# Kernel optimization log

Measured on AMD Instinct MI355X. Metric: run time of the kernel, lower is better.

## Reference

```python
import jax, jax.numpy as jnp
import numpy as np


def setup_inputs() -> dict:
    key = jax.random.key(0)
    ks = jax.random.split(key, 8)
    B, S, H = 8, 2048, 1024
    rep = jax.random.normal(ks[0], (B, S, H), dtype=jnp.float32)
    mask = jax.random.randint(ks[1], (B, S), 0, 2, dtype=jnp.int32)
    Ws = jax.random.normal(ks[2], (H, 2), dtype=jnp.float32) * 0.02
    bs = jax.random.normal(ks[3], (2,), dtype=jnp.float32) * 0.02
    We = jax.random.normal(ks[4], (H, 2), dtype=jnp.float32) * 0.02
    be = jax.random.normal(ks[5], (2,), dtype=jnp.float32) * 0.02
    Wm = jax.random.normal(ks[6], (4, 1), dtype=jnp.float32)
    bm = jax.random.normal(ks[7], (1,), dtype=jnp.float32)
    return {"rep": rep, "mask": mask, "Ws": Ws, "bs": bs, "We": We, "be": be, "Wm": Wm, "bm": bm}


def reference(rep, mask, Ws, bs, We, be, Wm, bm):
    # rep: [B,S,H]; start/end logits: [B,S,2]
    start_logits = rep @ Ws + bs
    end_logits = rep @ We + be
    maskb = mask != 0
    # candidate starts/ends: masked positions where logit[1] >= logit[0]
    start_cand = maskb & (start_logits[..., 0] <= start_logits[..., 1])  # [B,S]
    end_cand = maskb & (end_logits[..., 0] <= end_logits[..., 1])        # [B,S]
    # pair score m(cat(start_logits[b,s], end_logits[b,e])) decomposes additively
    w_start, w_end = Wm[:2, 0], Wm[2:, 0]
    score_s = start_logits @ w_start  # [B,S]
    score_e = end_logits @ w_end      # [B,S]
    pair_score = score_s[:, :, None] + score_e[:, None, :] + bm[0]  # [B,S,S]
    S = rep.shape[1]
    tri = jnp.arange(S)[:, None] <= jnp.arange(S)[None, :]  # s <= e
    valid = (start_cand[:, :, None] & end_cand[:, None, :] & tri & (pair_score > 0))  # [B,S,S]
    masked_scores = jnp.where(valid, pair_score, 0.0)
    return valid, masked_scores
```

## Files before the change

### kernel.cpp

```cpp
#include <hip/hip_runtime.h>

#define BB 8
#define SS 2048
#define HH 1024

__global__ __launch_bounds__(256) void token_kernel(
    const float* __restrict__ rep, const int* __restrict__ mask,
    const float* __restrict__ Ws, const float* __restrict__ bs,
    const float* __restrict__ We, const float* __restrict__ be,
    const float* __restrict__ Wm, const float* __restrict__ bm,
    float* __restrict__ ss, float* __restrict__ se)
{
    const int token = blockIdx.x * 4 + (threadIdx.x >> 6);
    const int lane  = threadIdx.x & 63;
    const float* r = rep + (size_t)token * HH;

    double a0 = 0.0, a1 = 0.0, a2 = 0.0, a3 = 0.0;
    #pragma unroll
    for (int k = 0; k < HH / 256; ++k) {
        const int h = k * 256 + lane * 4;
        const float4 rv = *(const float4*)(r + h);
        const float4 w0 = *(const float4*)(Ws + 2 * h);
        const float4 w1 = *(const float4*)(Ws + 2 * h + 4);
        const float4 e0 = *(const float4*)(We + 2 * h);
        const float4 e1 = *(const float4*)(We + 2 * h + 4);
        a0 += (double)rv.x * w0.x + (double)rv.y * w0.z + (double)rv.z * w1.x + (double)rv.w * w1.z;
        a1 += (double)rv.x * w0.y + (double)rv.y * w0.w + (double)rv.z * w1.y + (double)rv.w * w1.w;
        a2 += (double)rv.x * e0.x + (double)rv.y * e0.z + (double)rv.z * e1.x + (double)rv.w * e1.z;
        a3 += (double)rv.x * e0.y + (double)rv.y * e0.w + (double)rv.z * e1.y + (double)rv.w * e1.w;
    }
    #pragma unroll
    for (int off = 32; off >= 1; off >>= 1) {
        a0 += __shfl_down(a0, off);
        a1 += __shfl_down(a1, off);
        a2 += __shfl_down(a2, off);
        a3 += __shfl_down(a3, off);
    }
    if (lane == 0) {
        const double sl0 = a0 + (double)bs[0];
        const double sl1 = a1 + (double)bs[1];
        const double el0 = a2 + (double)be[0];
        const double el1 = a3 + (double)be[1];
        const bool m  = (mask[token] != 0);
        const bool sc = m && (sl0 <= sl1);
        const bool ec = m && (el0 <= el1);
        const double sv = sl0 * (double)Wm[0] + sl1 * (double)Wm[1];
        const double ev = el0 * (double)Wm[2] + el1 * (double)Wm[3];
        ss[token] = sc ? (float)sv : -1e30f;
        se[token] = ec ? (float)ev : -1e30f;
    }
}

__global__ __launch_bounds__(256) void pair_kernel(
    const float* __restrict__ ss, const float* __restrict__ se,
    const float* __restrict__ bm,
    float* __restrict__ out_valid, float* __restrict__ out_score)
{
    const int b = blockIdx.z;
    const int i = blockIdx.y;
    const int j = (blockIdx.x * 256 + threadIdx.x) * 4;

    const float s_i = ss[b * SS + i];
    const float4 e  = *(const float4*)(se + b * SS + j);
    const float bmv = bm[0];

    const float p0 = (s_i + e.x) + bmv;
    const float p1 = (s_i + e.y) + bmv;
    const float p2 = (s_i + e.z) + bmv;
    const float p3 = (s_i + e.w) + bmv;

    const bool v0 = (i <= j    ) && (p0 > 0.0f);
    const bool v1 = (i <= j + 1) && (p1 > 0.0f);
    const bool v2 = (i <= j + 2) && (p2 > 0.0f);
    const bool v3 = (i <= j + 3) && (p3 > 0.0f);

    const float4 vv = make_float4(v0 ? 1.0f : 0.0f, v1 ? 1.0f : 0.0f,
                                  v2 ? 1.0f : 0.0f, v3 ? 1.0f : 0.0f);
    const float4 pv = make_float4(v0 ? p0 : 0.0f, v1 ? p1 : 0.0f,
                                  v2 ? p2 : 0.0f, v3 ? p3 : 0.0f);

    const size_t off = ((size_t)b * SS + i) * SS + j;
    *(float4*)(out_valid + off) = vv;
    *(float4*)(out_score + off) = pv;
}

extern "C" void kernel_launch(void* const* d_in, const int* in_sizes, int n_in,
                              void* d_out, int out_size, void* d_ws, size_t ws_size,
                              hipStream_t stream) {
    const float* rep  = (const float*)d_in[0];
    const int*   mask = (const int*)  d_in[1];
    const float* Ws   = (const float*)d_in[2];
    const float* bs   = (const float*)d_in[3];
    const float* We   = (const float*)d_in[4];
    const float* be   = (const float*)d_in[5];
    const float* Wm   = (const float*)d_in[6];
    const float* bm   = (const float*)d_in[7];

    float* ss = (float*)d_ws;
    float* se = ss + BB * SS;

    float* out_valid = (float*)d_out;
    float* out_score = out_valid + (size_t)BB * SS * SS;

    token_kernel<<<BB * SS / 4, 256, 0, stream>>>(rep, mask, Ws, bs, We, be,
                                                  Wm, bm, ss, se);

    dim3 g2(SS / 1024, SS, BB);
    pair_kernel<<<g2, 256, 0, stream>>>(ss, se, bm, out_valid, out_score);
}
```

Before: 326.4 us.

## Multi-row pair tiles with nontemporal stores and register-cached weights in token kernel

The pair kernel now has each block cover 8 full rows: each thread loads 8 end scores once and writes 8 columns per row with nontemporal vector stores. This cuts block count and keeps the large streaming output from polluting caches. The token kernel has each wave handle 4 tokens, with the projection weights kept in registers and reused across them. The cost is higher register pressure and fewer blocks for latency hiding.

```diff
diff --git a/kernel.cpp b/kernel.cpp
--- a/kernel.cpp
+++ b/kernel.cpp
@@ -3,6 +3,8 @@
 #define BB 8
 #define SS 2048
 #define HH 1024
+
+typedef float vf4 __attribute__((ext_vector_type(4)));
 
 __global__ __launch_bounds__(256) void token_kernel(
     const float* __restrict__ rep, const int* __restrict__ mask,
@@ -11,43 +13,56 @@
     const float* __restrict__ Wm, const float* __restrict__ bm,
     float* __restrict__ ss, float* __restrict__ se)
 {
-    const int token = blockIdx.x * 4 + (threadIdx.x >> 6);
-    const int lane  = threadIdx.x & 63;
-    const float* r = rep + (size_t)token * HH;
+    const int wave = threadIdx.x >> 6;
+    const int lane = threadIdx.x & 63;
+    const int tok0 = blockIdx.x * 16 + wave * 4;
 
-    double a0 = 0.0, a1 = 0.0, a2 = 0.0, a3 = 0.0;
+    float4 w0[4], w1[4], e0[4], e1[4];
     #pragma unroll
-    for (int k = 0; k < HH / 256; ++k) {
+    for (int k = 0; k < 4; ++k) {
         const int h = k * 256 + lane * 4;
-        const float4 rv = *(const float4*)(r + h);
-        const float4 w0 = *(const float4*)(Ws + 2 * h);
-        const float4 w1 = *(const float4*)(Ws + 2 * h + 4);
-        const float4 e0 = *(const float4*)(We + 2 * h);
-        const float4 e1 = *(const float4*)(We + 2 * h + 4);
-        a0 += (double)rv.x * w0.x + (double)rv.y * w0.z + (double)rv.z * w1.x + (double)rv.w * w1.z;
-        a1 += (double)rv.x * w0.y + (double)rv.y * w0.w + (double)rv.z * w1.y + (double)rv.w * w1.w;
-        a2 += (double)rv.x * e0.x + (double)rv.y * e0.z + (double)rv.z * e1.x + (double)rv.w * e1.z;
-        a3 += (double)rv.x * e0.y + (double)rv.y * e0.w + (double)rv.z * e1.y + (double)rv.w * e1.w;
+        w0[k] = *(const float4*)(Ws + 2 * h);
+        w1[k] = *(const float4*)(Ws + 2 * h + 4);
+        e0[k] = *(const float4*)(We + 2 * h);
+        e1[k] = *(const float4*)(We + 2 * h + 4);
     }
+
     #pragma unroll
-    for (int off = 32; off >= 1; off >>= 1) {
-        a0 += __shfl_down(a0, off);
-        a1 += __shfl_down(a1, off);
-        a2 += __shfl_down(a2, off);
-        a3 += __shfl_down(a3, off);
-    }
-    if (lane == 0) {
-        const double sl0 = a0 + (double)bs[0];
-        const double sl1 = a1 + (double)bs[1];
-        const double el0 = a2 + (double)be[0];
-        const double el1 = a3 + (double)be[1];
-        const bool m  = (mask[token] != 0);
-        const bool sc = m && (sl0 <= sl1);
-        const bool ec = m && (el0 <= el1);
-        const double sv = sl0 * (double)Wm[0] + sl1 * (double)Wm[1];
-        const double ev = el0 * (double)Wm[2] + el1 * (double)Wm[3];
-        ss[token] = sc ? (float)sv : -1e30f;
-        se[token] = ec ? (float)ev : -1e30f;
+    for (int t = 0; t < 4; ++t) {
+        const int token = tok0 + t;
+        const float* r = rep + (size_t)token * HH;
+
+        double a0 = 0.0, a1 = 0.0, a2 = 0.0, a3 = 0.0;
+        #pragma unroll
+        for (int k = 0; k < 4; ++k) {
+            const float4 rv = *(const float4*)(r + k * 256 + lane * 4);
+            a0 += (double)rv.x * w0[k].x + (double)rv.y * w0[k].z + (double)rv.z * w1[k].x + (double)rv.w * w1[k].z;
+            a1 += (double)rv.x * w0[k].y + (double)rv.y * w0[k].w + (double)rv.z * w1[k].y + (double)rv.w * w1[k].w;
+            a2 += (double)rv.x * e0[k].x + (double)rv.y * e0[k].z + (double)rv.z * e1[k].x + (double)rv.w * e1[k].z;
+            a3 += (double)rv.x * e0[k].y + (double)rv.y * e0[k].w + (double)rv.z * e1[k].y + (double)rv.w * e1[k].w;
+        }
+
+        #pragma unroll
+        for (int off = 32; off >= 1; off >>= 1) {
+            a0 += __shfl_down(a0, off);
+            a1 += __shfl_down(a1, off);
+            a2 += __shfl_down(a2, off);
+            a3 += __shfl_down(a3, off);
+        }
+
+        if (lane == 0) {
+            const double sl0 = a0 + (double)bs[0];
+            const double sl1 = a1 + (double)bs[1];
+            const double el0 = a2 + (double)be[0];
+            const double el1 = a3 + (double)be[1];
+            const bool m  = (mask[token] != 0);
+            const bool sc = m && (sl0 <= sl1);
+            const bool ec = m && (el0 <= el1);
+            const double sv = sl0 * (double)Wm[0] + sl1 * (double)Wm[1];
+            const double ev = el0 * (double)Wm[2] + el1 * (double)Wm[3];
+            ss[token] = sc ? (float)sv : -1e30f;
+            se[token] = ec ? (float)ev : -1e30f;
+        }
     }
 }
 
@@ -56,32 +71,40 @@
     const float* __restrict__ bm,
     float* __restrict__ out_valid, float* __restrict__ out_score)
 {
-    const int b = blockIdx.z;
-    const int i = blockIdx.y;
-    const int j = (blockIdx.x * 256 + threadIdx.x) * 4;
-
-    const float s_i = ss[b * SS + i];
-    const float4 e  = *(const float4*)(se + b * SS + j);
+    const int row0 = blockIdx.x * 8;
+    const int b    = row0 >> 11;
+    const int j0   = threadIdx.x * 8;
     const float bmv = bm[0];
 
-    const float p0 = (s_i + e.x) + bmv;
-    const float p1 = (s_i + e.y) + bmv;
-    const float p2 = (s_i + e.z) + bmv;
-    const float p3 = (s_i + e.w) + bmv;
+    const float4 e0 = *(const float4*)(se + b * SS + j0);
+    const float4 e1 = *(const float4*)(se + b * SS + j0 + 4);
+    const float ev[8] = {e0.x, e0.y, e0.z, e0.w, e1.x, e1.y, e1.z, e1.w};
 
-    const bool v0 = (i <= j    ) && (p0 > 0.0f);
-    const bool v1 = (i <= j + 1) && (p1 > 0.0f);
-    const bool v2 = (i <= j + 2) && (p2 > 0.0f);
-    const bool v3 = (i <= j + 3) && (p3 > 0.0f);
+    #pragma unroll
+    for (int r = 0; r < 8; ++r) {
+        const int row = row0 + r;
+        const int i   = row & (SS - 1);
+        const float s_i = ss[row];
 
-    const float4 vv = make_float4(v0 ? 1.0f : 0.0f, v1 ? 1.0f : 0.0f,
-                                  v2 ? 1.0f : 0.0f, v3 ? 1.0f : 0.0f);
-    const float4 pv = make_float4(v0 ? p0 : 0.0f, v1 ? p1 : 0.0f,
-                                  v2 ? p2 : 0.0f, v3 ? p3 : 0.0f);
+        float va[8], pa[8];
+        #pragma unroll
+        for (int c = 0; c < 8; ++c) {
+            const float p = (s_i + ev[c]) + bmv;
+            const bool  v = (i <= j0 + c) && (p > 0.0f);
+            va[c] = v ? 1.0f : 0.0f;
+            pa[c] = v ? p    : 0.0f;
+        }
 
-    const size_t off = ((size_t)b * SS + i) * SS + j;
-    *(float4*)(out_valid + off) = vv;
-    *(float4*)(out_score + off) = pv;
+        const size_t off = (size_t)row * SS + j0;
+        vf4 vv0 = {va[0], va[1], va[2], va[3]};
+        vf4 vv1 = {va[4], va[5], va[6], va[7]};
+        vf4 pv0 = {pa[0], pa[1], pa[2], pa[3]};
+        vf4 pv1 = {pa[4], pa[5], pa[6], pa[7]};
+        __builtin_nontemporal_store(vv0, (vf4*)(out_valid + off));
+        __builtin_nontemporal_store(vv1, (vf4*)(out_valid + off + 4));
+        __builtin_nontemporal_store(pv0, (vf4*)(out_score + off));
+        __builtin_nontemporal_store(pv1, (vf4*)(out_score + off + 4));
+    }
 }
 
 extern "C" void kernel_launch(void* const* d_in, const int* in_sizes, int n_in,
@@ -102,9 +125,9 @@
     float* out_valid = (float*)d_out;
     float* out_score = out_valid + (size_t)BB * SS * SS;
 
-    token_kernel<<<BB * SS / 4, 256, 0, stream>>>(rep, mask, Ws, bs, We, be,
-                                                  Wm, bm, ss, se);
+    token_kernel<<<BB * SS / 16, 256, 0, stream>>>(rep, mask, Ws, bs, We, be,
+                                                   Wm, bm, ss, se);
 
-    dim3 g2(SS / 1024, SS, BB);
-    pair_kernel<<<g2, 256, 0, stream>>>(ss, se, bm, out_valid, out_score);
+    pair_kernel<<<BB * SS / 8, 256, 0, stream>>>(ss, se, bm,
+                                                 out_valid, out_score);
 }
```

Result: slower. 415.6 us (+27.3%).
